# Kernel tuning notes

Hardware: AMD Instinct MI355X
Metric: run time of the kernel (lower is better)

The kernel has to match this reference:

```python
import jax, jax.numpy as jnp
import numpy as np

H = 16          # num_heads
D = 64          # head_dim = dim // num_heads
ROPE_THETA = 10000.0
NEG = -1e9


def _rope_angles(n, d):
    # matches get_1d_rotary_pos_embed(head_dim, N): freqs_cis = polar(1, t outer (theta^-(2i/d)))
    inv_freq = 1.0 / (ROPE_THETA ** (jnp.arange(0, d, 2, dtype=jnp.float32) / d))  # [d/2]
    ang = jnp.arange(n, dtype=jnp.float32)[:, None] * inv_freq[None, :]            # [n, d/2]
    return jnp.cos(ang), jnp.sin(ang)


def _apply_rope(x, cos, sin):
    # x: [B,H,N,D]; complex rotation on adjacent pairs (use_real=False semantics)
    x0 = x[..., 0::2]
    x1 = x[..., 1::2]
    # broadcast cos/sin [N, D/2] over batch and heads
    r0 = x0 * cos - x1 * sin
    r1 = x0 * sin + x1 * cos
    return jnp.stack([r0, r1], axis=-1).reshape(x.shape)


def setup_inputs() -> dict:
    key = jax.random.key(0)
    ks = jax.random.split(key, 5)
    B, N, C = 4, 2048, 1024
    s_in = 1.0 / np.sqrt(C)
    return {
        "x": jax.random.normal(ks[0], (B, N, C), dtype=jnp.float32),
        "Wqkv_w": jax.random.normal(ks[1], (3 * C, C), dtype=jnp.float32) * s_in,
        "Wqkv_b": jax.random.normal(ks[2], (3 * C,), dtype=jnp.float32) * 0.01,
        "out_w": jax.random.normal(ks[3], (C, C), dtype=jnp.float32) * s_in,
        "out_b": jax.random.normal(ks[4], (C,), dtype=jnp.float32) * 0.01,
    }


def reference(x, Wqkv_w, Wqkv_b, out_w, out_b):
    B, N, C = x.shape
    scale = D ** -0.5
    # fused QKV projection: [B,N,3C] -> [3,B,H,N,D]
    qkv = (jnp.einsum('bnc,oc->bno', x, Wqkv_w) + Wqkv_b)
    qkv = qkv.reshape(B, N, 3, H, D).transpose(2, 0, 3, 1, 4)
    q, k, v = qkv[0], qkv[1], qkv[2]
    # qk_norm=False -> Identity
    cos, sin = _rope_angles(N, D)
    q = _apply_rope(q, cos, sin)
    k = _apply_rope(k, cos, sin)
    attn = jnp.einsum('bhqd,bhkd->bhqk', q * scale, k)      # [B,H,N,N]
    causal = jnp.triu(jnp.ones((N, N), dtype=bool), k=1)
    attn = jnp.where(causal[None, None], NEG, attn)
    attn = jax.nn.softmax(attn, axis=-1)
    o = jnp.einsum('bhqk,bhkd->bhqd', attn, v)              # [B,H,N,D]
    o = o.transpose(0, 2, 1, 3).reshape(B, N, C)
    return jnp.einsum('bnc,oc->bno', o, out_w) + out_b
```

## Files before the change

kernel.cpp:

```cpp
#include <hip/hip_runtime.h>
#include <hip/hip_bf16.h>

#define DEVI __device__ __forceinline__

typedef __attribute__((ext_vector_type(8))) short short8v;
typedef __attribute__((ext_vector_type(4))) float f32x4;
typedef __attribute__((ext_vector_type(2))) unsigned u32x2;

DEVI short f2bf(float f) {
  __hip_bfloat16 h = __float2bfloat16(f);
  return __builtin_bit_cast(short, h);
}
DEVI float bf2f(short s) {
  unsigned u = ((unsigned)(unsigned short)s) << 16;
  return __builtin_bit_cast(float, u);
}
DEVI unsigned packbf(float a, float b) {
  return (unsigned)(unsigned short)f2bf(a) | ((unsigned)(unsigned short)f2bf(b) << 16);
}
DEVI void gload16(const void* g, void* l) {
  __builtin_amdgcn_global_load_lds((const __attribute__((address_space(1))) void*)g,
                                   (__attribute__((address_space(3))) void*)l, 16, 0, 0);
}
#define MFMA16(a, b, c) __builtin_amdgcn_mfma_f32_16x16x32_bf16((a), (b), (c), 0, 0, 0)


__global__ void cvt_all(const float* __restrict__ x, const float* __restrict__ wq,
                        const float* __restrict__ wo, short* __restrict__ xb,
                        short* __restrict__ wqb, short* __restrict__ wob) {
  int i = blockIdx.x * blockDim.x + threadIdx.x;
  const float* in;
  short* out;
  if (i < 2097152) { in = x; out = xb; }
  else if (i < 2097152 + 786432) { in = wq; out = wqb; i -= 2097152; }
  else { in = wo; out = wob; i -= 2097152 + 786432; }
  float4 v = ((const float4*)in)[i];
  short4 o;
  o.x = f2bf(v.x); o.y = f2bf(v.y); o.z = f2bf(v.z); o.w = f2bf(v.w);
  ((short4*)out)[i] = o;
}

__global__ void rope_table(float2* __restrict__ tbl) {
  int i = blockIdx.x * blockDim.x + threadIdx.x;
  int n = i >> 5, f = i & 31;
  float inv = powf(10000.0f, -(float)f * (1.0f / 32.0f));
  float ang = (float)n * inv;
  tbl[i] = make_float2(cosf(ang), sinf(ang));
}

__global__ void rope_k(short* __restrict__ kk, const float2* __restrict__ tbl) {
  int i = blockIdx.x * blockDim.x + threadIdx.x;
  int row = i >> 3, c8 = i & 7;
  int n = row & 2047;
  short* ad = kk + (size_t)row * 64 + c8 * 8;
  short8v vv = *(short8v*)ad;
  short8v ov;
#pragma unroll
  for (int j = 0; j < 4; ++j) {
    float2 cs = tbl[n * 32 + c8 * 4 + j];
    float x0 = bf2f(vv[2 * j]), x1 = bf2f(vv[2 * j + 1]);
    ov[2 * j]     = f2bf(x0 * cs.x - x1 * cs.y);
    ov[2 * j + 1] = f2bf(x0 * cs.y + x1 * cs.x);
  }
  *(short8v*)ad = ov;
}

template <int EPI>
__global__ __launch_bounds__(256)
void gemm_bt(const short* __restrict__ A, const short* __restrict__ Bw,
             const float* __restrict__ bias,
             short* __restrict__ q, short* __restrict__ k, short* __restrict__ v,
             float* __restrict__ fout, int Mdim, int Ndim, int Kdim) {
  __shared__ __attribute__((aligned(16))) short As[3][128 * 32];
  __shared__ __attribute__((aligned(16))) short Bs[3][128 * 32];
  const int t = threadIdx.x;
  const int lane = t & 63, w = t >> 6;
  const int wr = w >> 1, wc = w & 1;
  const int g = lane >> 4, r16 = lane & 15;
  const int m0 = blockIdx.y * 128, n0 = blockIdx.x * 128;

  int goffs[2], loffs[2];
#pragma unroll
  for (int p = 0; p < 2; ++p) {
    int c = p * 256 + t;
    int row = c >> 2, u = c & 3;
    goffs[p] = row * Kdim + ((u ^ ((row >> 1) & 3)) * 8);
    loffs[p] = c * 16;
  }
  const short* Abase = A + (size_t)m0 * Kdim;
  const short* Bbase = Bw + (size_t)n0 * Kdim;

  auto STAGE = [&](int s, int k0) {
#pragma unroll
    for (int p = 0; p < 2; ++p) {
      gload16(Abase + k0 + goffs[p], (char*)&As[s][0] + loffs[p]);
      gload16(Bbase + k0 + goffs[p], (char*)&Bs[s][0] + loffs[p]);
    }
  };

  f32x4 acc[4][4];
#pragma unroll
  for (int i = 0; i < 4; ++i)
#pragma unroll
    for (int j = 0; j < 4; ++j) acc[i][j] = (f32x4){0.f, 0.f, 0.f, 0.f};

  const int nsteps = Kdim >> 5;
  STAGE(0, 0);
  STAGE(1, 32);
  asm volatile("s_waitcnt vmcnt(4)" ::: "memory");
  __builtin_amdgcn_s_barrier();
  asm volatile("" ::: "memory");

  int cur = 0, pre = 2;
  const int rsw = (r16 >> 1) & 3;
  for (int st = 0; st < nsteps; ++st) {
    if (st + 2 < nsteps) STAGE(pre, (st + 2) << 5);
    short8v af[4], bf[4];
#pragma unroll
    for (int mi = 0; mi < 4; ++mi)
      af[mi] = *(const short8v*)&As[cur][(wr * 64 + mi * 16 + r16) * 32 +
                                         ((g ^ rsw) * 8)];
#pragma unroll
    for (int ni = 0; ni < 4; ++ni)
      bf[ni] = *(const short8v*)&Bs[cur][(wc * 64 + ni * 16 + r16) * 32 +
                                         ((g ^ rsw) * 8)];
#pragma unroll
    for (int mi = 0; mi < 4; ++mi)
#pragma unroll
      for (int ni = 0; ni < 4; ++ni)
        acc[mi][ni] = MFMA16(af[mi], bf[ni], acc[mi][ni]);
    if (st + 2 < nsteps) asm volatile("s_waitcnt vmcnt(4)" ::: "memory");
    else                 asm volatile("s_waitcnt vmcnt(0)" ::: "memory");
    __builtin_amdgcn_s_barrier();
    asm volatile("" ::: "memory");
    cur = (cur == 2) ? 0 : cur + 1;
    pre = (pre == 2) ? 0 : pre + 1;
  }

  if (EPI == 0) {
    if (n0 >= 2048) {
      __shared__ __attribute__((aligned(16))) short Cs[64][136];
      const int b = m0 >> 11;
      const int nb = m0 & 2047;
#pragma unroll
      for (int hh = 0; hh < 2; ++hh) {
        if (wc == hh) {
#pragma unroll
          for (int ni = 0; ni < 4; ++ni) {
            float bv = bias[n0 + hh * 64 + ni * 16 + r16];
#pragma unroll
            for (int mi = 0; mi < 4; ++mi) {
              u32x2 pk;
              pk[0] = packbf(acc[mi][ni][0] + bv, acc[mi][ni][1] + bv);
              pk[1] = packbf(acc[mi][ni][2] + bv, acc[mi][ni][3] + bv);
              *(u32x2*)&Cs[ni * 16 + r16][wr * 64 + mi * 16 + g * 4] = pk;
            }
          }
        }
        __syncthreads();
        const int hdr = ((n0 + hh * 64) & 1023) >> 6;
        short* vdst = v + ((size_t)(b * 16 + hdr)) * 64 * 2048;
#pragma unroll
        for (int j = 0; j < 4; ++j) {
          int chunk = j * 256 + t;
          int d = chunk >> 4, c16 = chunk & 15;
          short8v val = *(const short8v*)&Cs[d][c16 * 8];
          *(short8v*)(vdst + (size_t)d * 2048 + nb + c16 * 8) = val;
        }
        __syncthreads();
      }
    } else {
#pragma unroll
      for (int ni = 0; ni < 4; ++ni) {
        int col = n0 + wc * 64 + ni * 16 + r16;
        float bv = bias[col];
        int s = col >> 10, rr = col & 1023, h = rr >> 6, d = rr & 63;
        short* dst = (s == 0) ? q : k;
#pragma unroll
        for (int mi = 0; mi < 4; ++mi) {
          int mrow = m0 + wr * 64 + mi * 16 + g * 4;
#pragma unroll
          for (int r = 0; r < 4; ++r) {
            int m = mrow + r;
            int b = m >> 11, n = m & 2047;
            dst[(((size_t)(b * 16 + h)) * 2048 + n) * 64 + d] = f2bf(acc[mi][ni][r] + bv);
          }
        }
      }
    }
  } else {
#pragma unroll
    for (int ni = 0; ni < 4; ++ni) {
      int col = n0 + wc * 64 + ni * 16 + r16;
      float bv = bias[col];
#pragma unroll
      for (int mi = 0; mi < 4; ++mi) {
        int mrow = m0 + wr * 64 + mi * 16 + g * 4;
#pragma unroll
        for (int r = 0; r < 4; ++r)
          fout[(size_t)(mrow + r) * Ndim + col] = acc[mi][ni][r] + bv;
      }
    }
  }
}

__global__ __launch_bounds__(256)
void fattn(const short* __restrict__ q, const short* __restrict__ k,
           const short* __restrict__ vT, const float2* __restrict__ tbl,
           short* __restrict__ o) {
  const int bx = blockIdx.x;
  const int qt = 15 - (bx >> 6);
  const int bh = bx & 63;
  const int b = bh >> 4, h = bh & 15;
  const int t = threadIdx.x, lane = t & 63, w = t >> 6;
  const int g = lane >> 4, r16 = lane & 15;

  __shared__ __attribute__((aligned(16))) short Ks[2][64 * 64];
  __shared__ __attribute__((aligned(16))) short Vt[2][64 * 64];
  __shared__ __attribute__((aligned(16))) short Ps[4][2][16 * 72];

  const short* qb = q + (size_t)bh * 2048 * 64;
  const short* kb = k + (size_t)bh * 2048 * 64;
  const short* vb = vT + (size_t)bh * 2048 * 64;

  int koffs[2], voffs[2], loffs[2];
#pragma unroll
  for (int p = 0; p < 2; ++p) {
    int c = p * 256 + t;
    int row = c >> 3, u = c & 7;
    int x8 = (u ^ (row & 7)) * 8;
    koffs[p] = row * 64 + x8;
    voffs[p] = row * 2048 + x8;
    loffs[p] = c * 16;
  }
  auto STAGE = [&](int s, int kt) {
#pragma unroll
    for (int p = 0; p < 2; ++p) {
      gload16(kb + (size_t)kt * 4096 + koffs[p], (char*)&Ks[s][0] + loffs[p]);
      gload16(vb + kt * 64 + voffs[p], (char*)&Vt[s][0] + loffs[p]);
    }
  };

  const int q0 = qt * 128 + w * 32;

  const float sc = 0.125f * 1.44269504088896f;
  short8v aq[2][2];
#pragma unroll
  for (int qi = 0; qi < 2; ++qi) {
    const int n = q0 + qi * 16 + r16;
#pragma unroll
    for (int dk = 0; dk < 2; ++dk) {
      short8v raw = *(const short8v*)(qb + (size_t)n * 64 + dk * 32 + g * 8);
      short8v rq;
#pragma unroll
      for (int j = 0; j < 4; ++j) {
        float2 cs = tbl[n * 32 + dk * 16 + g * 4 + j];
        float x0 = bf2f(raw[2 * j]), x1 = bf2f(raw[2 * j + 1]);
        rq[2 * j]     = f2bf((x0 * cs.x - x1 * cs.y) * sc);
        rq[2 * j + 1] = f2bf((x0 * cs.y + x1 * cs.x) * sc);
      }
      aq[qi][dk] = rq;
    }
  }

  const short one_bf = 0x3F80;
  const short8v ones = {one_bf, one_bf, one_bf, one_bf, one_bf, one_bf, one_bf, one_bf};
  const float M = 24.0f;

  f32x4 oacc[2][4], lacc[2];
#pragma unroll
  for (int qi = 0; qi < 2; ++qi) {
#pragma unroll
    for (int dc = 0; dc < 4; ++dc) oacc[qi][dc] = (f32x4){0.f, 0.f, 0.f, 0.f};
    lacc[qi] = (f32x4){0.f, 0.f, 0.f, 0.f};
  }

  const int ktmax = 2 * qt + 1;

  STAGE(0, 0);
  __syncthreads();

  for (int kt = 0; kt <= ktmax; ++kt) {
    const int cur = kt & 1;
    if (kt < ktmax) STAGE(cur ^ 1, kt + 1);

    const bool act0 = (kt * 64 <= q0 + 15);
    const bool act1 = (kt * 64 <= q0 + 31);

    f32x4 s[2][4];
#pragma unroll
    for (int qi = 0; qi < 2; ++qi)
#pragma unroll
      for (int kc = 0; kc < 4; ++kc) s[qi][kc] = (f32x4){0.f, 0.f, 0.f, 0.f};

    if (act1) {
      __builtin_amdgcn_s_setprio(1);
#pragma unroll
      for (int kc = 0; kc < 4; ++kc) {
        int key = kc * 16 + r16;
        const char* rb = (const char*)&Ks[cur][0] + key * 128;
        short8v kf0 = *(const short8v*)(rb + (((g) ^ (key & 7)) << 4));
        short8v kf1 = *(const short8v*)(rb + (((4 + g) ^ (key & 7)) << 4));
        if (act0) {
          s[0][kc] = MFMA16(kf0, aq[0][0], s[0][kc]);
          s[0][kc] = MFMA16(kf1, aq[0][1], s[0][kc]);
        }
        s[1][kc] = MFMA16(kf0, aq[1][0], s[1][kc]);
        s[1][kc] = MFMA16(kf1, aq[1][1], s[1][kc]);
      }
      __builtin_amdgcn_s_setprio(0);

#pragma unroll
      for (int qi = 0; qi < 2; ++qi) {
        if (qi == 0 && !act0) continue;
        const int qrow = q0 + qi * 16 + r16;
        const bool needmask = (kt * 64 + 63 > q0 + qi * 16);
        if (needmask) {
#pragma unroll
          for (int kc = 0; kc < 4; ++kc)
#pragma unroll
            for (int r = 0; r < 4; ++r)
              if (kt * 64 + kc * 16 + g * 4 + r > qrow) s[qi][kc][r] = -1e30f;
        }
        unsigned pk[4][2];
#pragma unroll
        for (int kc = 0; kc < 4; ++kc) {
          float p0 = __builtin_amdgcn_exp2f(s[qi][kc][0] - M);
          float p1 = __builtin_amdgcn_exp2f(s[qi][kc][1] - M);
          float p2 = __builtin_amdgcn_exp2f(s[qi][kc][2] - M);
          float p3 = __builtin_amdgcn_exp2f(s[qi][kc][3] - M);
          pk[kc][0] = packbf(p0, p1);
          pk[kc][1] = packbf(p2, p3);
        }
#pragma unroll
        for (int kc = 0; kc < 4; ++kc)
          *(u32x2*)((char*)&Ps[w][qi][0] + r16 * 144 + kc * 32 + g * 8) =
              (u32x2){pk[kc][0], pk[kc][1]};
      }

      asm volatile("" ::: "memory");

      short8v pa[2][2];
#pragma unroll
      for (int qi = 0; qi < 2; ++qi) {
        if (qi == 0 && !act0) continue;
#pragma unroll
        for (int kk = 0; kk < 2; ++kk)
          pa[qi][kk] =
              *(const short8v*)((char*)&Ps[w][qi][0] + r16 * 144 + kk * 64 + g * 16);
      }
      __builtin_amdgcn_s_setprio(1);
      if (act0) {
        lacc[0] = MFMA16(pa[0][0], ones, lacc[0]);
        lacc[0] = MFMA16(pa[0][1], ones, lacc[0]);
      }
      lacc[1] = MFMA16(pa[1][0], ones, lacc[1]);
      lacc[1] = MFMA16(pa[1][1], ones, lacc[1]);
#pragma unroll
      for (int dc = 0; dc < 4; ++dc) {
        int d = dc * 16 + r16;
        const char* vr = (const char*)&Vt[cur][0] + d * 128;
#pragma unroll
        for (int kk = 0; kk < 2; ++kk) {
          short8v bv = *(const short8v*)(vr + (((kk * 4 + g) ^ (d & 7)) << 4));
          if (act0) oacc[0][dc] = MFMA16(pa[0][kk], bv, oacc[0][dc]);
          oacc[1][dc] = MFMA16(pa[1][kk], bv, oacc[1][dc]);
        }
      }
      __builtin_amdgcn_s_setprio(0);
    }
    __syncthreads();
  }

#pragma unroll
  for (int qi = 0; qi < 2; ++qi) {
#pragma unroll
    for (int r = 0; r < 4; ++r) {
      float ilr = 1.f / lacc[qi][r];
      int qg = q0 + qi * 16 + g * 4 + r;
      short* orow = o + ((size_t)(b * 2048 + qg)) * 1024 + h * 64;
#pragma unroll
      for (int dc = 0; dc < 4; ++dc)
        orow[dc * 16 + r16] = f2bf(oacc[qi][dc][r] * ilr);
    }
  }
}

extern "C" void kernel_launch(void* const* d_in, const int* in_sizes, int n_in,
                              void* d_out, int out_size, void* d_ws, size_t ws_size,
                              hipStream_t stream) {
  const float* x    = (const float*)d_in[0];
  const float* Wqkv = (const float*)d_in[1];
  const float* bqkv = (const float*)d_in[2];
  const float* Wout = (const float*)d_in[3];
  const float* bout = (const float*)d_in[4];

  char* p = (char*)d_ws;
  short* xb = (short*)p;    p += (size_t)8192 * 1024 * 2;
  short* wqkvb = (short*)p; p += (size_t)3072 * 1024 * 2;
  short* woutb = (short*)p; p += (size_t)1024 * 1024 * 2;
  short* qbf = (short*)p;   p += (size_t)64 * 2048 * 64 * 2;
  short* kbf = (short*)p;   p += (size_t)64 * 2048 * 64 * 2;
  short* vbf = (short*)p;   p += (size_t)64 * 2048 * 64 * 2;
  float2* tbl = (float2*)p; p += (size_t)2048 * 32 * 8;

  cvt_all<<<12288, 256, 0, stream>>>(x, Wqkv, Wout, xb, wqkvb, woutb);
  rope_table<<<256, 256, 0, stream>>>(tbl);

  gemm_bt<0><<<dim3(24, 64), 256, 0, stream>>>(xb, wqkvb, bqkv, qbf, kbf, vbf, nullptr,
                                               8192, 3072, 1024);
  rope_k<<<4096, 256, 0, stream>>>(kbf, tbl);
  fattn<<<dim3(1024), 256, 0, stream>>>(qbf, kbf, vbf, tbl, xb);
  gemm_bt<1><<<dim3(8, 64), 256, 0, stream>>>(xb, woutb, bout, nullptr, nullptr, nullptr,
                                              (float*)d_out, 8192, 1024, 1024);
}
```

Baseline: 194.2 us.

## Use 256x256 tile, 512-thread kernel for QKV projection GEMM

Replaces the QKV projection GEMM with a dedicated kernel using 256x256 output tiles, 8 waves, and a 64-wide K step with double-buffered LDS and XOR swizzle. The larger tile raises arithmetic intensity and cuts global reloads of A and B. The V transpose epilogue now reuses the staging LDS. The output GEMM is split into its own f32-epilogue kernel. The trade-off is only 384 blocks, which may leave wave occupancy low and expose load latency with just two buffers.

After: 189.1 us. 1.03x faster.

```diff
diff --git a/kernel.cpp b/kernel.cpp
--- a/kernel.cpp
+++ b/kernel.cpp
@@ -65,12 +65,128 @@
   *(short8v*)ad = ov;
 }
 
-template <int EPI>
-__global__ __launch_bounds__(256)
-void gemm_bt(const short* __restrict__ A, const short* __restrict__ Bw,
+__global__ __launch_bounds__(512, 2)
+void gemm256(const short* __restrict__ A, const short* __restrict__ Bw,
              const float* __restrict__ bias,
              short* __restrict__ q, short* __restrict__ k, short* __restrict__ v,
-             float* __restrict__ fout, int Mdim, int Ndim, int Kdim) {
+             int Kdim) {
+  __shared__ __attribute__((aligned(16))) short lds[65536];
+  const int t = threadIdx.x;
+  const int lane = t & 63, w = t >> 6;
+  const int wr = w >> 2, wc = w & 3;
+  const int g = lane >> 4, r16 = lane & 15;
+  const int n0 = blockIdx.x * 256, m0 = blockIdx.y * 256;
+
+  int goffs[4], loffs[4];
+#pragma unroll
+  for (int p = 0; p < 4; ++p) {
+    int c = p * 512 + t;
+    int row = c >> 3, u = c & 7;
+    goffs[p] = row * Kdim + ((u ^ (row & 7)) * 8);
+    loffs[p] = c * 16;
+  }
+  const short* Abase = A + (size_t)m0 * Kdim;
+  const short* Bbase = Bw + (size_t)n0 * Kdim;
+
+  auto STAGE = [&](int s, int k0) {
+#pragma unroll
+    for (int p = 0; p < 4; ++p) {
+      gload16(Abase + k0 + goffs[p], (char*)lds + s * 32768 + loffs[p]);
+      gload16(Bbase + k0 + goffs[p], (char*)lds + 65536 + s * 32768 + loffs[p]);
+    }
+  };
+
+  f32x4 acc[8][4];
+#pragma unroll
+  for (int i = 0; i < 8; ++i)
+#pragma unroll
+    for (int j = 0; j < 4; ++j) acc[i][j] = (f32x4){0.f, 0.f, 0.f, 0.f};
+
+  const int nsteps = Kdim >> 6;
+  STAGE(0, 0);
+  __syncthreads();
+
+  int cur = 0;
+  for (int st = 0; st < nsteps; ++st) {
+    if (st + 1 < nsteps) STAGE(cur ^ 1, (st + 1) << 6);
+    const char* Ab = (const char*)lds + cur * 32768;
+    const char* Bb = (const char*)lds + 65536 + cur * 32768;
+#pragma unroll
+    for (int ks = 0; ks < 2; ++ks) {
+      short8v bf[4];
+#pragma unroll
+      for (int ni = 0; ni < 4; ++ni) {
+        int rowb = wc * 64 + ni * 16 + r16;
+        bf[ni] = *(const short8v*)(Bb + rowb * 128 + (((ks * 4 + g) ^ (rowb & 7)) << 4));
+      }
+#pragma unroll
+      for (int mi = 0; mi < 8; ++mi) {
+        int rowa = wr * 128 + mi * 16 + r16;
+        short8v af =
+            *(const short8v*)(Ab + rowa * 128 + (((ks * 4 + g) ^ (rowa & 7)) << 4));
+#pragma unroll
+        for (int ni = 0; ni < 4; ++ni)
+          acc[mi][ni] = MFMA16(af, bf[ni], acc[mi][ni]);
+      }
+    }
+    __syncthreads();
+    cur ^= 1;
+  }
+
+  const int b = m0 >> 11, nb = m0 & 2047;
+  if (n0 < 2048) {
+#pragma unroll
+    for (int ni = 0; ni < 4; ++ni) {
+      int col = n0 + wc * 64 + ni * 16 + r16;
+      float bv = bias[col];
+      int s = col >> 10, h = (col & 1023) >> 6, d = col & 63;
+      short* dst = (s == 0) ? q : k;
+#pragma unroll
+      for (int mi = 0; mi < 8; ++mi) {
+        int mrow = m0 + wr * 128 + mi * 16 + g * 4;
+#pragma unroll
+        for (int r = 0; r < 4; ++r) {
+          int n = (mrow + r) & 2047;
+          dst[(((size_t)(b * 16 + h)) * 2048 + n) * 64 + d] = f2bf(acc[mi][ni][r] + bv);
+        }
+      }
+    }
+  } else {
+    short* Cs = lds;
+    const int hdrb = (n0 - 2048) >> 6;
+#pragma unroll
+    for (int hh = 0; hh < 4; ++hh) {
+      if (wc == hh) {
+#pragma unroll
+        for (int ni = 0; ni < 4; ++ni) {
+          float bv = bias[n0 + hh * 64 + ni * 16 + r16];
+#pragma unroll
+          for (int mi = 0; mi < 8; ++mi) {
+            u32x2 pk;
+            pk[0] = packbf(acc[mi][ni][0] + bv, acc[mi][ni][1] + bv);
+            pk[1] = packbf(acc[mi][ni][2] + bv, acc[mi][ni][3] + bv);
+            *(u32x2*)&Cs[(ni * 16 + r16) * 264 + wr * 128 + mi * 16 + g * 4] = pk;
+          }
+        }
+      }
+      __syncthreads();
+      short* vdst = v + ((size_t)(b * 16 + hdrb + hh)) * 64 * 2048;
+#pragma unroll
+      for (int j = 0; j < 4; ++j) {
+        int chunk = j * 512 + t;
+        int d = chunk >> 5, c = chunk & 31;
+        short8v val = *(const short8v*)&Cs[d * 264 + c * 8];
+        *(short8v*)(vdst + (size_t)d * 2048 + nb + c * 8) = val;
+      }
+      __syncthreads();
+    }
+  }
+}
+
+__global__ __launch_bounds__(256)
+void gemm_f32(const short* __restrict__ A, const short* __restrict__ Bw,
+              const float* __restrict__ bias, float* __restrict__ fout,
+              int Ndim, int Kdim) {
   __shared__ __attribute__((aligned(16))) short As[3][128 * 32];
   __shared__ __attribute__((aligned(16))) short Bs[3][128 * 32];
   const int t = threadIdx.x;
@@ -137,69 +253,16 @@
     pre = (pre == 2) ? 0 : pre + 1;
   }
 
-  if (EPI == 0) {
-    if (n0 >= 2048) {
-      __shared__ __attribute__((aligned(16))) short Cs[64][136];
-      const int b = m0 >> 11;
-      const int nb = m0 & 2047;
-#pragma unroll
-      for (int hh = 0; hh < 2; ++hh) {
-        if (wc == hh) {
-#pragma unroll
-          for (int ni = 0; ni < 4; ++ni) {
-            float bv = bias[n0 + hh * 64 + ni * 16 + r16];
-#pragma unroll
-            for (int mi = 0; mi < 4; ++mi) {
-              u32x2 pk;
-              pk[0] = packbf(acc[mi][ni][0] + bv, acc[mi][ni][1] + bv);
-              pk[1] = packbf(acc[mi][ni][2] + bv, acc[mi][ni][3] + bv);
-              *(u32x2*)&Cs[ni * 16 + r16][wr * 64 + mi * 16 + g * 4] = pk;
-            }
-          }
-        }
-        __syncthreads();
-        const int hdr = ((n0 + hh * 64) & 1023) >> 6;
-        short* vdst = v + ((size_t)(b * 16 + hdr)) * 64 * 2048;
-#pragma unroll
-        for (int j = 0; j < 4; ++j) {
-          int chunk = j * 256 + t;
-          int d = chunk >> 4, c16 = chunk & 15;
-          short8v val = *(const short8v*)&Cs[d][c16 * 8];
-          *(short8v*)(vdst + (size_t)d * 2048 + nb + c16 * 8) = val;
-        }
-        __syncthreads();
-      }
-    } else {
-#pragma unroll
-      for (int ni = 0; ni < 4; ++ni) {
-        int col = n0 + wc * 64 + ni * 16 + r16;
-        float bv = bias[col];
-        int s = col >> 10, rr = col & 1023, h = rr >> 6, d = rr & 63;
-        short* dst = (s == 0) ? q : k;
-#pragma unroll
-        for (int mi = 0; mi < 4; ++mi) {
-          int mrow = m0 + wr * 64 + mi * 16 + g * 4;
-#pragma unroll
-          for (int r = 0; r < 4; ++r) {
-            int m = mrow + r;
-            int b = m >> 11, n = m & 2047;
-            dst[(((size_t)(b * 16 + h)) * 2048 + n) * 64 + d] = f2bf(acc[mi][ni][r] + bv);
-          }
-        }
-      }
-    }
-  } else {
-#pragma unroll
-    for (int ni = 0; ni < 4; ++ni) {
-      int col = n0 + wc * 64 + ni * 16 + r16;
-      float bv = bias[col];
-#pragma unroll
-      for (int mi = 0; mi < 4; ++mi) {
-        int mrow = m0 + wr * 64 + mi * 16 + g * 4;
-#pragma unroll
-        for (int r = 0; r < 4; ++r)
-          fout[(size_t)(mrow + r) * Ndim + col] = acc[mi][ni][r] + bv;
-      }
+#pragma unroll
+  for (int ni = 0; ni < 4; ++ni) {
+    int col = n0 + wc * 64 + ni * 16 + r16;
+    float bv = bias[col];
+#pragma unroll
+    for (int mi = 0; mi < 4; ++mi) {
+      int mrow = m0 + wr * 64 + mi * 16 + g * 4;
+#pragma unroll
+      for (int r = 0; r < 4; ++r)
+        fout[(size_t)(mrow + r) * Ndim + col] = acc[mi][ni][r] + bv;
     }
   }
 }
@@ -407,10 +470,8 @@
   cvt_all<<<12288, 256, 0, stream>>>(x, Wqkv, Wout, xb, wqkvb, woutb);
   rope_table<<<256, 256, 0, stream>>>(tbl);
 
-  gemm_bt<0><<<dim3(24, 64), 256, 0, stream>>>(xb, wqkvb, bqkv, qbf, kbf, vbf, nullptr,
-                                               8192, 3072, 1024);
+  gemm256<<<dim3(12, 32), 512, 0, stream>>>(xb, wqkvb, bqkv, qbf, kbf, vbf, 1024);
   rope_k<<<4096, 256, 0, stream>>>(kbf, tbl);
   fattn<<<dim3(1024), 256, 0, stream>>>(qbf, kbf, vbf, tbl, xb);
-  gemm_bt<1><<<dim3(8, 64), 256, 0, stream>>>(xb, woutb, bout, nullptr, nullptr, nullptr,
-                                              (float*)d_out, 8192, 1024, 1024);
-}
+  gemm_f32<<<dim3(8, 64), 256, 0, stream>>>(xb, woutb, bout, (float*)d_out, 1024, 1024);
+}
```
